# Kernel tuning notes

Hardware: AMD Instinct MI355X
Metric: run time of the kernel (lower is better)

The kernel has to match this reference:

```python
import jax, jax.numpy as jnp
import numpy as np

NUM_HEADS = 16
THETA = 10000.0


def _rope(x, cos, sin):
    # x: [B, H, S, d_k]; cos/sin: [S, d_k//2]
    x_even = x[..., 0::2]
    x_odd = x[..., 1::2]
    out_even = x_even * cos - x_odd * sin
    out_odd = x_odd * cos + x_even * sin
    # interleave back to original even/odd layout
    return jnp.stack([out_even, out_odd], axis=-1).reshape(x.shape)


def setup_inputs() -> dict:
    key = jax.random.key(0)
    ks = jax.random.split(key, 5)
    B, S, D = 2, 2048, 1024
    std = 2.0 / (D + D)
    return {
        "x": jax.random.normal(ks[0], (B, S, D), dtype=jnp.float32),
        "w_q": jax.random.normal(ks[1], (D, D), dtype=jnp.float32) * std,
        "w_k": jax.random.normal(ks[2], (D, D), dtype=jnp.float32) * std,
        "w_v": jax.random.normal(ks[3], (D, D), dtype=jnp.float32) * std,
        "w_o": jax.random.normal(ks[4], (D, D), dtype=jnp.float32) * std,
    }


def reference(x, w_q, w_k, w_v, w_o):
    B, S, D = x.shape
    H = NUM_HEADS
    d_k = D // H

    # QKV projections: x @ W.T
    q = jnp.einsum('bsd,ed->bse', x, w_q).reshape(B, S, H, d_k).transpose(0, 2, 1, 3)
    k = jnp.einsum('bsd,ed->bse', x, w_k).reshape(B, S, H, d_k).transpose(0, 2, 1, 3)
    v = jnp.einsum('bsd,ed->bse', x, w_v).reshape(B, S, H, d_k).transpose(0, 2, 1, 3)

    # RoPE (token_positions = arange(S))
    pos = jnp.arange(S, dtype=jnp.float32)
    inv_freq = 1.0 / (THETA ** (2.0 * jnp.arange(d_k // 2, dtype=jnp.float32) / d_k))
    angles = pos[:, None] * inv_freq[None, :]  # [S, d_k//2]
    cos, sin = jnp.cos(angles), jnp.sin(angles)
    q = _rope(q, cos, sin)
    k = _rope(k, cos, sin)

    # causal attention
    scores = jnp.einsum('bhqd,bhkd->bhqk', q, k) / jnp.sqrt(jnp.float32(d_k))
    causal = jnp.tril(jnp.ones((S, S), dtype=bool))
    scores = jnp.where(causal[None, None], scores, -jnp.inf)
    attn = jax.nn.softmax(scores, axis=-1)
    out = jnp.einsum('bhqk,bhkd->bhqd', attn, v)  # [B, H, S, d_k]

    out = out.transpose(0, 2, 1, 3).reshape(B, S, D)
    return jnp.einsum('bsd,ed->bse', out, w_o)
```

## Files before the change

### kernel.cpp

```cpp
#include <hip/hip_runtime.h>

typedef unsigned short u16;
typedef unsigned int u32;
typedef short bf16x8 __attribute__((ext_vector_type(8)));
typedef float f32x4 __attribute__((ext_vector_type(4)));

#define CSC 0.18033688011112042f

__device__ __forceinline__ u16 f2bf(float f) {
    union { float f; unsigned u; } x; x.f = f;
    unsigned r = x.u + 0x7fffu + ((x.u >> 16) & 1u);
    return (u16)(r >> 16);
}
__device__ __forceinline__ float bf2f(u16 v) {
    union { unsigned u; float f; } x; x.u = ((unsigned)v) << 16;
    return x.f;
}
__device__ __forceinline__ u32 cvt_pk_bf16(float lo, float hi) {
    u32 r;
    asm("v_cvt_pk_bf16_f32 %0, %1, %2" : "=v"(r) : "v"(lo), "v"(hi));
    return r;
}
__device__ __forceinline__ float exp2_fast(float x) {
#if __has_builtin(__builtin_amdgcn_exp2f)
    return __builtin_amdgcn_exp2f(x);
#else
    return exp2f(x);
#endif
}
__device__ __forceinline__ void gl_lds16(const u16* g, u16* l) {
#if __has_builtin(__builtin_amdgcn_global_load_lds)
    __builtin_amdgcn_global_load_lds(
        (const __attribute__((address_space(1))) unsigned int*)g,
        (__attribute__((address_space(3))) unsigned int*)l, 16, 0, 0);
#else
    *(bf16x8*)l = *(const bf16x8*)g;
#endif
}
__device__ __forceinline__ int ileave(int x) {
    return (x < 16) ? (x << 1) : (((x - 16) << 1) | 1);
}

__global__ void cvt_all_kernel(const float* __restrict__ x, const float* __restrict__ wq,
                               const float* __restrict__ wk, const float* __restrict__ wv,
                               const float* __restrict__ wo,
                               u16* __restrict__ xb, u16* __restrict__ qkvw,
                               u16* __restrict__ ow) {
    int i = blockIdx.x * 256 + threadIdx.x;
    const float4* src;
    ushort4* dst;
    if (i < 1048576) {
        src = (const float4*)x + i;
        dst = (ushort4*)xb + i;
    } else {
        int r = i - 1048576;
        int m = r >> 18;
        int off = r & 262143;
        const float* s4 = (m == 0) ? wq : (m == 1) ? wk : (m == 2) ? wv : wo;
        u16* d = (m < 3) ? (qkvw + (size_t)m * 1048576) : ow;
        src = (const float4*)s4 + off;
        dst = (ushort4*)d + off;
    }
    float4 v = *src;
    ushort4 o;
    o.x = f2bf(v.x); o.y = f2bf(v.y); o.z = f2bf(v.z); o.w = f2bf(v.w);
    *dst = o;
}

__global__ void rope_kernel(u16* __restrict__ qb, u16* __restrict__ kb) {
    int idx = blockIdx.x * 256 + threadIdx.x;
    u16* buf;
    float scale;
    if (blockIdx.y == 0) { buf = qb; scale = CSC; } else { buf = kb; scale = 1.0f; }
    int g   = idx & 7;
    int row = idx >> 3;
    int s   = row & 2047;
    u16* p = buf + (size_t)row * 64 + g * 8;
    bf16x8 v = *(bf16x8*)p;
    bf16x8 o;
    #pragma unroll
    for (int q = 0; q < 4; ++q) {
        int i = g * 4 + q;
        float inv = exp2_fast((float)i * -0.4152410118609203f);
        float ang = (float)s * inv;
        float sn, cs;
        sincosf(ang, &sn, &cs);
        float e  = bf2f(((u16*)&v)[2 * q]);
        float od = bf2f(((u16*)&v)[2 * q + 1]);
        ((u16*)&o)[2 * q]     = f2bf((e * cs - od * sn) * scale);
        ((u16*)&o)[2 * q + 1] = f2bf((od * cs + e * sn) * scale);
    }
    *(bf16x8*)p = o;
}

__global__ __launch_bounds__(256) void gemm_qkv(const u16* __restrict__ A,
                                                const u16* __restrict__ Bw,
                                                u16* __restrict__ C, int K) {
    __shared__ __align__(16) u16 SB[16384];
    u16* SH = SB;
    const int tid  = threadIdx.x;
    const int bm   = blockIdx.x * 128;
    const int bn   = blockIdx.y * 128;
    const int wave = tid >> 6, lane = tid & 63;
    const int wm   = (wave >> 1) * 64, wn = (wave & 1) * 64;
    const int l16  = lane & 15, quad = lane >> 4;
    const int mat  = bn >> 10;

    f32x4 acc[4][4];
    #pragma unroll
    for (int i = 0; i < 4; i++)
        #pragma unroll
        for (int j = 0; j < 4; j++)
            #pragma unroll
            for (int e = 0; e < 4; e++) acc[i][j][e] = 0.0f;

    const int srow = tid >> 2;
    const int scol = (((tid & 3) ^ ((tid >> 3) & 3))) * 8;
    const u16* gA0 = A  + (size_t)(bm + srow) * K + scol;
    const u16* gA1 = A  + (size_t)(bm + 64 + srow) * K + scol;
    const u16* gB0 = Bw + (size_t)(bn + srow) * K + scol;
    const u16* gB1 = Bw + (size_t)(bn + 64 + srow) * K + scol;
    const int csw = (quad ^ ((l16 >> 1) & 3)) * 8;

    auto stage = [&](int k0, int buf) {
        u16* As = SB + buf * 8192;
        u16* Bs = As + 4096;
        gl_lds16(gA0 + k0, As + (size_t)tid * 8);
        gl_lds16(gA1 + k0, As + (size_t)(tid + 256) * 8);
        gl_lds16(gB0 + k0, Bs + (size_t)tid * 8);
        gl_lds16(gB1 + k0, Bs + (size_t)(tid + 256) * 8);
    };

    stage(0, 0);
    int cur = 0;
    for (int k0 = 0; k0 < K; k0 += 32) {
        __syncthreads();
        if (k0 + 32 < K) stage(k0 + 32, cur ^ 1);
        const u16* As = SB + cur * 8192;
        const u16* Bs = As + 4096;
        bf16x8 af[4], bfr[4];
        #pragma unroll
        for (int i = 0; i < 4; i++) af[i]  = *(const bf16x8*)&As[(wm + i * 16 + l16) * 32 + csw];
        #pragma unroll
        for (int j = 0; j < 4; j++) bfr[j] = *(const bf16x8*)&Bs[(wn + j * 16 + l16) * 32 + csw];
        #pragma unroll
        for (int i = 0; i < 4; i++)
            #pragma unroll
            for (int j = 0; j < 4; j++)
                acc[i][j] = __builtin_amdgcn_mfma_f32_16x16x32_bf16(af[i], bfr[j], acc[i][j], 0, 0, 0);
        cur ^= 1;
    }

    const int b  = bm >> 11, sb = bm & 2047;
    if (mat < 2) {
        #pragma unroll
        for (int pass = 0; pass < 2; ++pass) {
            __syncthreads();
            if ((wn >> 6) == pass) {
                #pragma unroll
                for (int i = 0; i < 4; i++)
                    #pragma unroll
                    for (int j = 0; j < 4; j++)
                        #pragma unroll
                        for (int r = 0; r < 4; r++) {
                            int rl = wm + i * 16 + quad * 4 + r;
                            int cl = j * 16 + l16;
                            SH[rl * 66 + cl] = f2bf(acc[i][j][r]);
                        }
            }
            __syncthreads();
            int rl   = tid >> 1;
            int half = (tid & 1) * 32;
            int c    = (bn + pass * 64) & 1023;
            int h    = c >> 6;
            int s    = sb + rl;
            u16* dst = C + (size_t)mat * 4194304 +
                       (((size_t)(b * 16 + h) * 2048 + s) * 64) + half;
            const u16* srcp = &SH[rl * 66 + half];
            #pragma unroll
            for (int kk = 0; kk < 4; ++kk)
                *(bf16x8*)(dst + kk * 8) = *(const bf16x8*)(srcp + kk * 8);
        }
    } else {
        #pragma unroll
        for (int pass = 0; pass < 2; ++pass) {
            __syncthreads();
            if ((wn >> 6) == pass) {
                #pragma unroll
                for (int i = 0; i < 4; i++)
                    #pragma unroll
                    for (int j = 0; j < 4; j++)
                        #pragma unroll
                        for (int r = 0; r < 4; r++) {
                            int row = j * 16 + l16;
                            int ml  = wm + i * 16 + quad * 4 + r;
                            int sp  = (ml & ~31) | ileave(ml & 31);
                            SH[row * 130 + sp] = f2bf(acc[i][j][r]);
                        }
            }
            __syncthreads();
            int row = tid >> 2, seg = tid & 3;
            int cc  = (bn + pass * 64 + row) & 1023;
            int h = cc >> 6, dv = cc & 63;
            u16* dst = C + (size_t)8388608 +
                       (((size_t)(b * 16 + h) * 64 + dv) * 2048) + sb + seg * 32;
            const u16* srcp = &SH[row * 130 + seg * 32];
            #pragma unroll
            for (int kk = 0; kk < 4; ++kk)
                *(bf16x8*)(dst + kk * 8) = *(const bf16x8*)(srcp + kk * 8);
        }
    }
}

__global__ __launch_bounds__(256, 2) void gemm_out(const u16* __restrict__ A,
                                                   const u16* __restrict__ Bw,
                                                   float* __restrict__ C, int K) {
    __shared__ __align__(16) u16 SB[12288];
    const int tid  = threadIdx.x;
    const int bm   = blockIdx.x * 128;
    const int bn   = blockIdx.y * 64;
    const int wave = tid >> 6, lane = tid & 63;
    const int wm   = wave * 32;
    const int l16  = lane & 15, quad = lane >> 4;

    f32x4 acc[2][4];
    #pragma unroll
    for (int i = 0; i < 2; i++)
        #pragma unroll
        for (int j = 0; j < 4; j++)
            #pragma unroll
            for (int e = 0; e < 4; e++) acc[i][j][e] = 0.0f;

    const int srow = tid >> 2;
    const int scol = (((tid & 3) ^ ((tid >> 3) & 3))) * 8;
    const u16* gA0 = A  + (size_t)(bm + srow) * K + scol;
    const u16* gA1 = A  + (size_t)(bm + 64 + srow) * K + scol;
    const u16* gB0 = Bw + (size_t)(bn + srow) * K + scol;
    const int csw = (quad ^ ((l16 >> 1) & 3)) * 8;

    auto stage = [&](int k0, int buf) {
        u16* base = SB + buf * 6144;
        gl_lds16(gA0 + k0, base + (size_t)tid * 8);
        gl_lds16(gA1 + k0, base + (size_t)(tid + 256) * 8);
        gl_lds16(gB0 + k0, base + 4096 + (size_t)tid * 8);
    };

    stage(0, 0);
    int cur = 0;
    for (int k0 = 0; k0 < K; k0 += 32) {
        __syncthreads();
        if (k0 + 32 < K) stage(k0 + 32, cur ^ 1);
        const u16* As = SB + cur * 6144;
        const u16* Bs = As + 4096;
        bf16x8 af[2], bfr[4];
        #pragma unroll
        for (int i = 0; i < 2; i++) af[i]  = *(const bf16x8*)&As[(wm + i * 16 + l16) * 32 + csw];
        #pragma unroll
        for (int j = 0; j < 4; j++) bfr[j] = *(const bf16x8*)&Bs[(j * 16 + l16) * 32 + csw];
        #pragma unroll
        for (int i = 0; i < 2; i++)
            #pragma unroll
            for (int j = 0; j < 4; j++)
                acc[i][j] = __builtin_amdgcn_mfma_f32_16x16x32_bf16(af[i], bfr[j], acc[i][j], 0, 0, 0);
        cur ^= 1;
    }

    #pragma unroll
    for (int i = 0; i < 2; i++)
        #pragma unroll
        for (int j = 0; j < 4; j++)
            #pragma unroll
            for (int r = 0; r < 4; r++) {
                int mr = bm + wm + i * 16 + quad * 4 + r;
                int nc = bn + j * 16 + l16;
                C[(size_t)mr * 1024 + nc] = acc[i][j][r];
            }
}

__global__ __launch_bounds__(512, 2) void attn_kernel(const u16* __restrict__ Q,
                                                      const u16* __restrict__ Kb,
                                                      const u16* __restrict__ Vt,
                                                      u16* __restrict__ Oout) {
    __shared__ __align__(16) u16 KV[2][8192];
    __shared__ __align__(16) u16 PW[8 * 1024];
    const int tid  = threadIdx.x;
    const int wave = tid >> 6, lane = tid & 63;
    const int side = wave >> 2;
    const int wl   = wave & 3;
    const int l16  = lane & 15, quad = lane >> 4;
    const int bid  = blockIdx.x;
    const int j    = (bid >> 3) & 15;
    const int bh   = (bid & 7) * 4 + (bid >> 7);
    const int T    = 32 - j;
    const int q0   = (side == 0 ? (31 - j) : j) * 64 + wl * 16;
    const int dTil = (side == 0) ? (T - 1) : j;

    const u16* Qh = Q  + (size_t)bh * 2048 * 64;
    const u16* Kh = Kb + (size_t)bh * 2048 * 64;
    const u16* Vh = Vt + (size_t)bh * 64 * 2048;

    bf16x8 qf0 = *(const bf16x8*)&Qh[(size_t)(q0 + l16) * 64 + quad * 8];
    bf16x8 qf1 = *(const bf16x8*)&Qh[(size_t)(q0 + l16) * 64 + 32 + quad * 8];

    f32x4 o[4];
    float ls[4];
    #pragma unroll
    for (int t = 0; t < 4; t++)
        #pragma unroll
        for (int e = 0; e < 4; e++) o[t][e] = 0.0f;
    #pragma unroll
    for (int r = 0; r < 4; r++) ls[r] = 0.0f;

    const int tid2 = tid & 255;
    const int srow = tid2 >> 2;
    const int scs  = (((tid2 & 3) ^ ((tid2 >> 3) & 3))) * 8;
    const u16* gK = Kh + (size_t)srow * 64 + scs;
    const u16* gV = Vh + (size_t)srow * 2048 + scs;

    const int cswz = (quad ^ ((l16 >> 1) & 3)) * 8;
    const int psw0 = ((quad ^ (l16 & 7)) << 3);
    const int psw1 = (((quad ^ (l16 & 7)) ^ 4) << 3);

    u16* pw16 = PW + wave * 1024;
    u32* pw32 = (u32*)pw16;

    auto stage = [&](int t, int buf) {
        u16* base = KV[buf];
        if (tid < 256) {
            gl_lds16(gK + (size_t)t * 4096,      base + (size_t)tid2 * 8);
            gl_lds16(gK + (size_t)t * 4096 + 32, base + 2048 + (size_t)tid2 * 8);
        } else {
            gl_lds16(gV + (size_t)t * 64,        base + 4096 + (size_t)tid2 * 8);
            gl_lds16(gV + (size_t)t * 64 + 32,   base + 6144 + (size_t)tid2 * 8);
        }
    };

    stage(0, 0);
    for (int t = 0; t < T; ++t) {
        __syncthreads();
        if (t + 1 < T) stage(t + 1, (t + 1) & 1);
        const bool act = (side == 0) || (t <= j);
        if (act) {
            const u16* B = KV[t & 1];
            bf16x8 kf0[4], kf1[4], vf0[4], vf1[4];
            #pragma unroll
            for (int n = 0; n < 4; n++) {
                int ri = (n * 16 + l16) * 32 + cswz;
                kf0[n] = *(const bf16x8*)&B[ri];
                kf1[n] = *(const bf16x8*)&B[2048 + ri];
                vf0[n] = *(const bf16x8*)&B[4096 + ri];
                vf1[n] = *(const bf16x8*)&B[6144 + ri];
            }
            const int kbase = t * 64;
            const bool diag = (t == dTil);

            f32x4 s[4];
            #pragma unroll
            for (int n = 0; n < 4; n++) {
                #pragma unroll
                for (int e = 0; e < 4; e++) s[n][e] = 0.0f;
                s[n] = __builtin_amdgcn_mfma_f32_16x16x32_bf16(qf0, kf0[n], s[n], 0, 0, 0);
                s[n] = __builtin_amdgcn_mfma_f32_16x16x32_bf16(qf1, kf1[n], s[n], 0, 0, 0);
            }
            float p[4][4];
            #pragma unroll
            for (int n = 0; n < 4; n++)
                #pragma unroll
                for (int r = 0; r < 4; r++) {
                    float v = exp2_fast(s[n][r]);
                    if (diag) {
                        int row = q0 + quad * 4 + r;
                        v = (kbase + n * 16 + l16 > row) ? 0.0f : v;
                    }
                    p[n][r] = v;
                    ls[r] += v;
                }
            #pragma unroll
            for (int c = 0; c < 2; c++)
                #pragma unroll
                for (int r = 0; r < 4; r++) {
                    int prow = quad * 4 + r;
                    int pj   = (((c * 4 + (l16 >> 2)) ^ (prow & 7)) << 2) | (l16 & 3);
                    pw32[prow * 32 + pj] = cvt_pk_bf16(p[2 * c][r], p[2 * c + 1][r]);
                }
            asm volatile("s_waitcnt lgkmcnt(0)" ::: "memory");
            bf16x8 pf0 = *(const bf16x8*)&pw16[l16 * 64 + psw0];
            bf16x8 pf1 = *(const bf16x8*)&pw16[l16 * 64 + psw1];
            #pragma unroll
            for (int dn = 0; dn < 4; dn++) {
                o[dn] = __builtin_amdgcn_mfma_f32_16x16x32_bf16(pf0, vf0[dn], o[dn], 0, 0, 0);
                o[dn] = __builtin_amdgcn_mfma_f32_16x16x32_bf16(pf1, vf1[dn], o[dn], 0, 0, 0);
            }
        }
    }

    #pragma unroll
    for (int off = 1; off < 16; off <<= 1)
        #pragma unroll
        for (int r = 0; r < 4; r++)
            ls[r] += __shfl_xor(ls[r], off);

    const int b = bh >> 4, h = bh & 15;
    #pragma unroll
    for (int r = 0; r < 4; r++) {
        float inv = 1.0f / ls[r];
        int srw = q0 + quad * 4 + r;
        #pragma unroll
        for (int dn = 0; dn < 4; dn++) {
            int d = h * 64 + dn * 16 + l16;
            Oout[((size_t)b * 2048 + srw) * 1024 + d] = f2bf(o[dn][r] * inv);
        }
    }
}

extern "C" void kernel_launch(void* const* d_in, const int* in_sizes, int n_in,
                              void* d_out, int out_size, void* d_ws, size_t ws_size,
                              hipStream_t stream) {
    const float* x  = (const float*)d_in[0];
    const float* wq = (const float*)d_in[1];
    const float* wk = (const float*)d_in[2];
    const float* wv = (const float*)d_in[3];
    const float* wo = (const float*)d_in[4];
    float* out = (float*)d_out;

    const int M = 4096, D = 1024;
    u16* xb    = (u16*)d_ws;
    u16* qkvw  = xb   + (size_t)M * D;
    u16* ow    = qkvw + (size_t)3 * D * D;
    u16* qkv   = ow   + (size_t)D * D;
    u16* qb    = qkv;
    u16* kb    = qkv + (size_t)M * D;
    u16* vtb   = qkv + (size_t)2 * M * D;
    u16* aob   = qkv + (size_t)3 * M * D;

    cvt_all_kernel<<<8192, 256, 0, stream>>>(x, wq, wk, wv, wo, xb, qkvw, ow);

    dim3 gq(32, 24);
    gemm_qkv<<<gq, 256, 0, stream>>>(xb, qkvw, qkv, D);

    dim3 gr(2048, 2);
    rope_kernel<<<gr, 2048 ? 256 : 256, 0, stream>>>(qb, kb);

    attn_kernel<<<512, 512, 0, stream>>>(qb, kb, vtb, aob);

    dim3 go(32, 16);
    gemm_out<<<go, 256, 0, stream>>>(aob, ow, out, D);
}
```

Baseline: 179.1 us.

## Give each attention wave two 16-row query blocks and halve block size

The attention kernel now runs 256 threads per block with 4 waves instead of 8. Each wave handles 32 query rows (two 16-row blocks) rather than 16, so every K/V fragment read from LDS feeds twice as many MFMAs. All threads now stage both K and V. The aim is to cut LDS fragment traffic per FLOP and raise instruction-level parallelism, at the cost of more registers per wave and fewer waves for latency hiding.

```diff
diff --git a/kernel.cpp b/kernel.cpp
--- a/kernel.cpp
+++ b/kernel.cpp
@@ -277,43 +277,49 @@
             }
 }
 
-__global__ __launch_bounds__(512, 2) void attn_kernel(const u16* __restrict__ Q,
+__global__ __launch_bounds__(256, 2) void attn_kernel(const u16* __restrict__ Q,
                                                       const u16* __restrict__ Kb,
                                                       const u16* __restrict__ Vt,
                                                       u16* __restrict__ Oout) {
     __shared__ __align__(16) u16 KV[2][8192];
-    __shared__ __align__(16) u16 PW[8 * 1024];
+    __shared__ __align__(16) u16 PW[4 * 2048];
     const int tid  = threadIdx.x;
     const int wave = tid >> 6, lane = tid & 63;
-    const int side = wave >> 2;
-    const int wl   = wave & 3;
+    const int side = wave >> 1;
+    const int wl   = wave & 1;
     const int l16  = lane & 15, quad = lane >> 4;
     const int bid  = blockIdx.x;
     const int j    = (bid >> 3) & 15;
     const int bh   = (bid & 7) * 4 + (bid >> 7);
     const int T    = 32 - j;
-    const int q0   = (side == 0 ? (31 - j) : j) * 64 + wl * 16;
+    const int qt   = (side == 0) ? (31 - j) : j;
+    const int q0   = qt * 64 + wl * 32;
     const int dTil = (side == 0) ? (T - 1) : j;
 
     const u16* Qh = Q  + (size_t)bh * 2048 * 64;
     const u16* Kh = Kb + (size_t)bh * 2048 * 64;
     const u16* Vh = Vt + (size_t)bh * 64 * 2048;
 
-    bf16x8 qf0 = *(const bf16x8*)&Qh[(size_t)(q0 + l16) * 64 + quad * 8];
-    bf16x8 qf1 = *(const bf16x8*)&Qh[(size_t)(q0 + l16) * 64 + 32 + quad * 8];
-
-    f32x4 o[4];
-    float ls[4];
-    #pragma unroll
-    for (int t = 0; t < 4; t++)
-        #pragma unroll
-        for (int e = 0; e < 4; e++) o[t][e] = 0.0f;
-    #pragma unroll
-    for (int r = 0; r < 4; r++) ls[r] = 0.0f;
-
-    const int tid2 = tid & 255;
-    const int srow = tid2 >> 2;
-    const int scs  = (((tid2 & 3) ^ ((tid2 >> 3) & 3))) * 8;
+    bf16x8 qf[2][2];
+    #pragma unroll
+    for (int rb = 0; rb < 2; rb++) {
+        qf[rb][0] = *(const bf16x8*)&Qh[(size_t)(q0 + rb * 16 + l16) * 64 + quad * 8];
+        qf[rb][1] = *(const bf16x8*)&Qh[(size_t)(q0 + rb * 16 + l16) * 64 + 32 + quad * 8];
+    }
+
+    f32x4 o[2][4];
+    float ls[2][4];
+    #pragma unroll
+    for (int rb = 0; rb < 2; rb++)
+        #pragma unroll
+        for (int dn = 0; dn < 4; dn++) {
+            #pragma unroll
+            for (int e = 0; e < 4; e++) o[rb][dn][e] = 0.0f;
+            ls[rb][dn] = 0.0f;
+        }
+
+    const int srow = tid >> 2;
+    const int scs  = (((tid & 3) ^ ((tid >> 3) & 3))) * 8;
     const u16* gK = Kh + (size_t)srow * 64 + scs;
     const u16* gV = Vh + (size_t)srow * 2048 + scs;
 
@@ -321,18 +327,14 @@
     const int psw0 = ((quad ^ (l16 & 7)) << 3);
     const int psw1 = (((quad ^ (l16 & 7)) ^ 4) << 3);
 
-    u16* pw16 = PW + wave * 1024;
-    u32* pw32 = (u32*)pw16;
+    u16* pw16 = PW + wave * 2048;
 
     auto stage = [&](int t, int buf) {
         u16* base = KV[buf];
-        if (tid < 256) {
-            gl_lds16(gK + (size_t)t * 4096,      base + (size_t)tid2 * 8);
-            gl_lds16(gK + (size_t)t * 4096 + 32, base + 2048 + (size_t)tid2 * 8);
-        } else {
-            gl_lds16(gV + (size_t)t * 64,        base + 4096 + (size_t)tid2 * 8);
-            gl_lds16(gV + (size_t)t * 64 + 32,   base + 6144 + (size_t)tid2 * 8);
-        }
+        gl_lds16(gK + (size_t)t * 4096,      base + (size_t)tid * 8);
+        gl_lds16(gK + (size_t)t * 4096 + 32, base + 2048 + (size_t)tid * 8);
+        gl_lds16(gV + (size_t)t * 64,        base + 4096 + (size_t)tid * 8);
+        gl_lds16(gV + (size_t)t * 64 + 32,   base + 6144 + (size_t)tid * 8);
     };
 
     stage(0, 0);
@@ -354,63 +356,75 @@
             const int kbase = t * 64;
             const bool diag = (t == dTil);
 
-            f32x4 s[4];
-            #pragma unroll
-            for (int n = 0; n < 4; n++) {
-                #pragma unroll
-                for (int e = 0; e < 4; e++) s[n][e] = 0.0f;
-                s[n] = __builtin_amdgcn_mfma_f32_16x16x32_bf16(qf0, kf0[n], s[n], 0, 0, 0);
-                s[n] = __builtin_amdgcn_mfma_f32_16x16x32_bf16(qf1, kf1[n], s[n], 0, 0, 0);
-            }
-            float p[4][4];
-            #pragma unroll
-            for (int n = 0; n < 4; n++)
-                #pragma unroll
-                for (int r = 0; r < 4; r++) {
-                    float v = exp2_fast(s[n][r]);
-                    if (diag) {
-                        int row = q0 + quad * 4 + r;
-                        v = (kbase + n * 16 + l16 > row) ? 0.0f : v;
+            #pragma unroll
+            for (int rb = 0; rb < 2; rb++) {
+                f32x4 s[4];
+                #pragma unroll
+                for (int n = 0; n < 4; n++) {
+                    #pragma unroll
+                    for (int e = 0; e < 4; e++) s[n][e] = 0.0f;
+                    s[n] = __builtin_amdgcn_mfma_f32_16x16x32_bf16(qf[rb][0], kf0[n], s[n], 0, 0, 0);
+                    s[n] = __builtin_amdgcn_mfma_f32_16x16x32_bf16(qf[rb][1], kf1[n], s[n], 0, 0, 0);
+                }
+                float p[4][4];
+                #pragma unroll
+                for (int n = 0; n < 4; n++)
+                    #pragma unroll
+                    for (int r = 0; r < 4; r++) {
+                        float v = exp2_fast(s[n][r]);
+                        if (diag) {
+                            int row = q0 + rb * 16 + quad * 4 + r;
+                            v = (kbase + n * 16 + l16 > row) ? 0.0f : v;
+                        }
+                        p[n][r] = v;
+                        ls[rb][r] += v;
                     }
-                    p[n][r] = v;
-                    ls[r] += v;
+                u32* pw32 = (u32*)(pw16 + rb * 1024);
+                #pragma unroll
+                for (int c = 0; c < 2; c++)
+                    #pragma unroll
+                    for (int r = 0; r < 4; r++) {
+                        int prow = quad * 4 + r;
+                        int pj   = (((c * 4 + (l16 >> 2)) ^ (prow & 7)) << 2) | (l16 & 3);
+                        pw32[prow * 32 + pj] = cvt_pk_bf16(p[2 * c][r], p[2 * c + 1][r]);
+                    }
+            }
+            asm volatile("s_waitcnt lgkmcnt(0)" ::: "memory");
+            #pragma unroll
+            for (int rb = 0; rb < 2; rb++) {
+                const u16* pp = pw16 + rb * 1024;
+                bf16x8 pf0 = *(const bf16x8*)&pp[l16 * 64 + psw0];
+                bf16x8 pf1 = *(const bf16x8*)&pp[l16 * 64 + psw1];
+                #pragma unroll
+                for (int dn = 0; dn < 4; dn++) {
+                    o[rb][dn] = __builtin_amdgcn_mfma_f32_16x16x32_bf16(pf0, vf0[dn], o[rb][dn], 0, 0, 0);
+                    o[rb][dn] = __builtin_amdgcn_mfma_f32_16x16x32_bf16(pf1, vf1[dn], o[rb][dn], 0, 0, 0);
                 }
-            #pragma unroll
-            for (int c = 0; c < 2; c++)
-                #pragma unroll
-                for (int r = 0; r < 4; r++) {
-                    int prow = quad * 4 + r;
-                    int pj   = (((c * 4 + (l16 >> 2)) ^ (prow & 7)) << 2) | (l16 & 3);
-                    pw32[prow * 32 + pj] = cvt_pk_bf16(p[2 * c][r], p[2 * c + 1][r]);
-                }
-            asm volatile("s_waitcnt lgkmcnt(0)" ::: "memory");
-            bf16x8 pf0 = *(const bf16x8*)&pw16[l16 * 64 + psw0];
-            bf16x8 pf1 = *(const bf16x8*)&pw16[l16 * 64 + psw1];
+            }
+        }
+    }
+
+    #pragma unroll
+    for (int off = 1; off < 16; off <<= 1)
+        #pragma unroll
+        for (int rb = 0; rb < 2; rb++)
+            #pragma unroll
+            for (int r = 0; r < 4; r++)
+                ls[rb][r] += __shfl_xor(ls[rb][r], off);
+
+    const int b = bh >> 4, h = bh & 15;
+    #pragma unroll
+    for (int rb = 0; rb < 2; rb++)
+        #pragma unroll
+        for (int r = 0; r < 4; r++) {
+            float inv = 1.0f / ls[rb][r];
+            int srw = q0 + rb * 16 + quad * 4 + r;
             #pragma unroll
             for (int dn = 0; dn < 4; dn++) {
-                o[dn] = __builtin_amdgcn_mfma_f32_16x16x32_bf16(pf0, vf0[dn], o[dn], 0, 0, 0);
-                o[dn] = __builtin_amdgcn_mfma_f32_16x16x32_bf16(pf1, vf1[dn], o[dn], 0, 0, 0);
+                int d = h * 64 + dn * 16 + l16;
+                Oout[((size_t)b * 2048 + srw) * 1024 + d] = f2bf(o[rb][dn][r] * inv);
             }
         }
-    }
-
-    #pragma unroll
-    for (int off = 1; off < 16; off <<= 1)
-        #pragma unroll
-        for (int r = 0; r < 4; r++)
-            ls[r] += __shfl_xor(ls[r], off);
-
-    const int b = bh >> 4, h = bh & 15;
-    #pragma unroll
-    for (int r = 0; r < 4; r++) {
-        float inv = 1.0f / ls[r];
-        int srw = q0 + quad * 4 + r;
-        #pragma unroll
-        for (int dn = 0; dn < 4; dn++) {
-            int d = h * 64 + dn * 16 + l16;
-            Oout[((size_t)b * 2048 + srw) * 1024 + d] = f2bf(o[dn][r] * inv);
-        }
-    }
 }
 
 extern "C" void kernel_launch(void* const* d_in, const int* in_sizes, int n_in,
@@ -439,9 +453,9 @@
     gemm_qkv<<<gq, 256, 0, stream>>>(xb, qkvw, qkv, D);
 
     dim3 gr(2048, 2);
-    rope_kernel<<<gr, 2048 ? 256 : 256, 0, stream>>>(qb, kb);
-
-    attn_kernel<<<512, 512, 0, stream>>>(qb, kb, vtb, aob);
+    rope_kernel<<<gr, 256, 0, stream>>>(qb, kb);
+
+    attn_kernel<<<512, 256, 0, stream>>>(qb, kb, vtb, aob);
 
     dim3 go(32, 16);
     gemm_out<<<go, 256, 0, stream>>>(aob, ow, out, D);
```

Result: slower. 193.1 us (+7.8%).

## Fuse RoPE into QKV GEMM epilogue and raise wave priority around attention MFMAs

Applied to the files above, without the earlier changes.

Removes the standalone RoPE kernel and applies the rotary embedding and Q scaling inside the QKV GEMM epilogue, while the tile sits in LDS before the store. This avoids one launch and a full read-modify-write pass over Q and K in global memory. It also wraps the attention MFMA blocks in s_setprio so matrix issue gets priority over other waves. The cost is extra sincos work in the GEMM epilogue, which may lengthen its tail.

```diff
diff --git a/kernel.cpp b/kernel.cpp
--- a/kernel.cpp
+++ b/kernel.cpp
@@ -67,32 +67,6 @@
     *dst = o;
 }
 
-__global__ void rope_kernel(u16* __restrict__ qb, u16* __restrict__ kb) {
-    int idx = blockIdx.x * 256 + threadIdx.x;
-    u16* buf;
-    float scale;
-    if (blockIdx.y == 0) { buf = qb; scale = CSC; } else { buf = kb; scale = 1.0f; }
-    int g   = idx & 7;
-    int row = idx >> 3;
-    int s   = row & 2047;
-    u16* p = buf + (size_t)row * 64 + g * 8;
-    bf16x8 v = *(bf16x8*)p;
-    bf16x8 o;
-    #pragma unroll
-    for (int q = 0; q < 4; ++q) {
-        int i = g * 4 + q;
-        float inv = exp2_fast((float)i * -0.4152410118609203f);
-        float ang = (float)s * inv;
-        float sn, cs;
-        sincosf(ang, &sn, &cs);
-        float e  = bf2f(((u16*)&v)[2 * q]);
-        float od = bf2f(((u16*)&v)[2 * q + 1]);
-        ((u16*)&o)[2 * q]     = f2bf((e * cs - od * sn) * scale);
-        ((u16*)&o)[2 * q + 1] = f2bf((od * cs + e * sn) * scale);
-    }
-    *(bf16x8*)p = o;
-}
-
 __global__ __launch_bounds__(256) void gemm_qkv(const u16* __restrict__ A,
                                                 const u16* __restrict__ Bw,
                                                 u16* __restrict__ C, int K) {
@@ -153,6 +127,7 @@
 
     const int b  = bm >> 11, sb = bm & 2047;
     if (mat < 2) {
+        const float scale = (mat == 0) ? CSC : 1.0f;
         #pragma unroll
         for (int pass = 0; pass < 2; ++pass) {
             __syncthreads();
@@ -177,9 +152,25 @@
             u16* dst = C + (size_t)mat * 4194304 +
                        (((size_t)(b * 16 + h) * 2048 + s) * 64) + half;
             const u16* srcp = &SH[rl * 66 + half];
-            #pragma unroll
-            for (int kk = 0; kk < 4; ++kk)
-                *(bf16x8*)(dst + kk * 8) = *(const bf16x8*)(srcp + kk * 8);
+            const int ibase = half >> 1;
+            #pragma unroll
+            for (int kk = 0; kk < 4; ++kk) {
+                bf16x8 v = *(const bf16x8*)(srcp + kk * 8);
+                bf16x8 ov;
+                #pragma unroll
+                for (int q = 0; q < 4; ++q) {
+                    int i = ibase + kk * 4 + q;
+                    float inv = exp2_fast((float)i * -0.4152410118609203f);
+                    float ang = (float)s * inv;
+                    float sn, cs;
+                    sincosf(ang, &sn, &cs);
+                    float e  = bf2f(((u16*)&v)[2 * q]);
+                    float od = bf2f(((u16*)&v)[2 * q + 1]);
+                    ((u16*)&ov)[2 * q]     = f2bf((e * cs - od * sn) * scale);
+                    ((u16*)&ov)[2 * q + 1] = f2bf((od * cs + e * sn) * scale);
+                }
+                *(bf16x8*)(dst + kk * 8) = ov;
+            }
         }
     } else {
         #pragma unroll
@@ -355,6 +346,7 @@
             const bool diag = (t == dTil);
 
             f32x4 s[4];
+            __builtin_amdgcn_s_setprio(1);
             #pragma unroll
             for (int n = 0; n < 4; n++) {
                 #pragma unroll
@@ -362,6 +354,7 @@
                 s[n] = __builtin_amdgcn_mfma_f32_16x16x32_bf16(qf0, kf0[n], s[n], 0, 0, 0);
                 s[n] = __builtin_amdgcn_mfma_f32_16x16x32_bf16(qf1, kf1[n], s[n], 0, 0, 0);
             }
+            __builtin_amdgcn_s_setprio(0);
             float p[4][4];
             #pragma unroll
             for (int n = 0; n < 4; n++)
@@ -386,11 +379,13 @@
             asm volatile("s_waitcnt lgkmcnt(0)" ::: "memory");
             bf16x8 pf0 = *(const bf16x8*)&pw16[l16 * 64 + psw0];
             bf16x8 pf1 = *(const bf16x8*)&pw16[l16 * 64 + psw1];
+            __builtin_amdgcn_s_setprio(1);
             #pragma unroll
             for (int dn = 0; dn < 4; dn++) {
                 o[dn] = __builtin_amdgcn_mfma_f32_16x16x32_bf16(pf0, vf0[dn], o[dn], 0, 0, 0);
                 o[dn] = __builtin_amdgcn_mfma_f32_16x16x32_bf16(pf1, vf1[dn], o[dn], 0, 0, 0);
             }
+            __builtin_amdgcn_s_setprio(0);
         }
     }
 
@@ -438,9 +433,6 @@
     dim3 gq(32, 24);
     gemm_qkv<<<gq, 256, 0, stream>>>(xb, qkvw, qkv, D);
 
-    dim3 gr(2048, 2);
-    rope_kernel<<<gr, 2048 ? 256 : 256, 0, stream>>>(qb, kb);
-
     attn_kernel<<<512, 512, 0, stream>>>(qb, kb, vtb, aob);
 
     dim3 go(32, 16);
```

Measured after the change: 178.7 us. About the same (-0.2%).

## Deepen gemm_out K-tile to 64 with XOR swizzle; raise MFMA wave priority in attention

Applied to the files above, without the earlier changes.

The output-projection GEMM now stages 64-wide K slices instead of 32, with a new 8-way XOR swizzle in LDS, so it runs half as many barrier iterations and issues more MFMAs per sync. The attention kernel wraps its QK and PV MFMA blocks in s_setprio so waves issuing matrix ops are scheduled ahead of others. The GEMM change doubles its LDS footprint to 48KB, which may cut occupancy. The rope launch expression is also tidied to a plain 256.

```diff
diff --git a/kernel.cpp b/kernel.cpp
--- a/kernel.cpp
+++ b/kernel.cpp
@@ -215,7 +215,7 @@
 __global__ __launch_bounds__(256, 2) void gemm_out(const u16* __restrict__ A,
                                                    const u16* __restrict__ Bw,
                                                    float* __restrict__ C, int K) {
-    __shared__ __align__(16) u16 SB[12288];
+    __shared__ __align__(16) u16 SB[24576];
     const int tid  = threadIdx.x;
     const int bm   = blockIdx.x * 128;
     const int bn   = blockIdx.y * 64;
@@ -231,37 +231,44 @@
             #pragma unroll
             for (int e = 0; e < 4; e++) acc[i][j][e] = 0.0f;
 
-    const int srow = tid >> 2;
-    const int scol = (((tid & 3) ^ ((tid >> 3) & 3))) * 8;
-    const u16* gA0 = A  + (size_t)(bm + srow) * K + scol;
-    const u16* gA1 = A  + (size_t)(bm + 64 + srow) * K + scol;
-    const u16* gB0 = Bw + (size_t)(bn + srow) * K + scol;
-    const int csw = (quad ^ ((l16 >> 1) & 3)) * 8;
+    const int srowS = tid >> 3;
+    const int scol8 = (((tid & 7) ^ ((tid >> 3) & 7))) * 8;
+    const u16* gA = A  + (size_t)(bm + srowS) * K + scol8;
+    const u16* gB = Bw + (size_t)(bn + srowS) * K + scol8;
+    const int rsw = (l16 & 7);
 
     auto stage = [&](int k0, int buf) {
-        u16* base = SB + buf * 6144;
-        gl_lds16(gA0 + k0, base + (size_t)tid * 8);
-        gl_lds16(gA1 + k0, base + (size_t)(tid + 256) * 8);
-        gl_lds16(gB0 + k0, base + 4096 + (size_t)tid * 8);
+        u16* As = SB + buf * 12288;
+        u16* Bs = As + 8192;
+        #pragma unroll
+        for (int l = 0; l < 4; ++l)
+            gl_lds16(gA + (size_t)(l * 32) * K + k0, As + (size_t)(l * 256 + tid) * 8);
+        #pragma unroll
+        for (int l = 0; l < 2; ++l)
+            gl_lds16(gB + (size_t)(l * 32) * K + k0, Bs + (size_t)(l * 256 + tid) * 8);
     };
 
     stage(0, 0);
     int cur = 0;
-    for (int k0 = 0; k0 < K; k0 += 32) {
+    for (int k0 = 0; k0 < K; k0 += 64) {
         __syncthreads();
-        if (k0 + 32 < K) stage(k0 + 32, cur ^ 1);
-        const u16* As = SB + cur * 6144;
-        const u16* Bs = As + 4096;
-        bf16x8 af[2], bfr[4];
-        #pragma unroll
-        for (int i = 0; i < 2; i++) af[i]  = *(const bf16x8*)&As[(wm + i * 16 + l16) * 32 + csw];
-        #pragma unroll
-        for (int j = 0; j < 4; j++) bfr[j] = *(const bf16x8*)&Bs[(j * 16 + l16) * 32 + csw];
-        #pragma unroll
-        for (int i = 0; i < 2; i++)
-            #pragma unroll
-            for (int j = 0; j < 4; j++)
-                acc[i][j] = __builtin_amdgcn_mfma_f32_16x16x32_bf16(af[i], bfr[j], acc[i][j], 0, 0, 0);
+        if (k0 + 64 < K) stage(k0 + 64, cur ^ 1);
+        const u16* As = SB + cur * 12288;
+        const u16* Bs = As + 8192;
+        #pragma unroll
+        for (int kk = 0; kk < 2; ++kk) {
+            const int ch = ((kk * 4 + quad) ^ rsw) * 8;
+            bf16x8 af[2], bfr[4];
+            #pragma unroll
+            for (int i = 0; i < 2; i++) af[i]  = *(const bf16x8*)&As[(wm + i * 16 + l16) * 64 + ch];
+            #pragma unroll
+            for (int j = 0; j < 4; j++) bfr[j] = *(const bf16x8*)&Bs[(j * 16 + l16) * 64 + ch];
+            #pragma unroll
+            for (int i = 0; i < 2; i++)
+                #pragma unroll
+                for (int j = 0; j < 4; j++)
+                    acc[i][j] = __builtin_amdgcn_mfma_f32_16x16x32_bf16(af[i], bfr[j], acc[i][j], 0, 0, 0);
+        }
         cur ^= 1;
     }
 
@@ -355,6 +362,7 @@
             const bool diag = (t == dTil);
 
             f32x4 s[4];
+            __builtin_amdgcn_s_setprio(1);
             #pragma unroll
             for (int n = 0; n < 4; n++) {
                 #pragma unroll
@@ -362,6 +370,7 @@
                 s[n] = __builtin_amdgcn_mfma_f32_16x16x32_bf16(qf0, kf0[n], s[n], 0, 0, 0);
                 s[n] = __builtin_amdgcn_mfma_f32_16x16x32_bf16(qf1, kf1[n], s[n], 0, 0, 0);
             }
+            __builtin_amdgcn_s_setprio(0);
             float p[4][4];
             #pragma unroll
             for (int n = 0; n < 4; n++)
@@ -386,11 +395,13 @@
             asm volatile("s_waitcnt lgkmcnt(0)" ::: "memory");
             bf16x8 pf0 = *(const bf16x8*)&pw16[l16 * 64 + psw0];
             bf16x8 pf1 = *(const bf16x8*)&pw16[l16 * 64 + psw1];
+            __builtin_amdgcn_s_setprio(1);
             #pragma unroll
             for (int dn = 0; dn < 4; dn++) {
                 o[dn] = __builtin_amdgcn_mfma_f32_16x16x32_bf16(pf0, vf0[dn], o[dn], 0, 0, 0);
                 o[dn] = __builtin_amdgcn_mfma_f32_16x16x32_bf16(pf1, vf1[dn], o[dn], 0, 0, 0);
             }
+            __builtin_amdgcn_s_setprio(0);
         }
     }
 
@@ -439,7 +450,7 @@
     gemm_qkv<<<gq, 256, 0, stream>>>(xb, qkvw, qkv, D);
 
     dim3 gr(2048, 2);
-    rope_kernel<<<gr, 2048 ? 256 : 256, 0, stream>>>(qb, kb);
+    rope_kernel<<<gr, 256, 0, stream>>>(qb, kb);
 
     attn_kernel<<<512, 512, 0, stream>>>(qb, kb, vtb, aob);
 
```

Result: no change. 178.1 us (-0.6%).
